# Optimization experiments

Measured on AMD Instinct MI355X. Metric: run time of the kernel, lower is better.

## Reference

```python
import jax, jax.numpy as jnp
import numpy as np

B, T, N, D = 16, 12, 2048, 128  # T*D == 12*hidden_dim, D == hidden_dim (structural constraint)


def _lin(key, out_dim, in_dim):
    k1, k2 = jax.random.split(key)
    s = 1.0 / np.sqrt(in_dim)
    W = jax.random.uniform(k1, (out_dim, in_dim), jnp.float32, -s, s)
    b = jax.random.uniform(k2, (out_dim,), jnp.float32, -s, s)
    return W, b


def setup_inputs() -> dict:
    key = jax.random.key(0)
    ks = jax.random.split(key, 12)
    x = jax.random.normal(ks[0], (B, T, N, D), jnp.float32)
    Wd1, bd1 = _lin(ks[1], D, 12 * D)      # conv_down[0] (1x1 conv == linear over channels)
    Wd2, bd2 = _lin(ks[2], D, D)           # conv_down[3]
    Wq, bq = _lin(ks[3], D, D)
    Wk, bk = _lin(ks[4], D, D)
    Wv, bv = _lin(ks[5], D, D)
    Wu1, bu1 = _lin(ks[6], 12 * D, D)      # conv_up[0]
    Wu2, bu2 = _lin(ks[7], 12 * D, 12 * D) # conv_up[3]
    gamma = jnp.ones((D,), jnp.float32)
    beta = jnp.zeros((D,), jnp.float32)
    Wr1, br1 = _lin(ks[8], D, D)
    Wr2, br2 = _lin(ks[9], D, D)
    Wi1, bi1 = _lin(ks[10], D, D)
    Wi2, bi2 = _lin(ks[11], D, D)
    return dict(x=x, Wd1=Wd1, bd1=bd1, Wd2=Wd2, bd2=bd2, Wq=Wq, bq=bq, Wk=Wk, bk=bk,
                Wv=Wv, bv=bv, Wu1=Wu1, bu1=bu1, Wu2=Wu2, bu2=bu2, gamma=gamma, beta=beta,
                Wr1=Wr1, br1=br1, Wr2=Wr2, br2=br2, Wi1=Wi1, bi1=bi1, Wi2=Wi2, bi2=bi2)


def _mlp(x, W1, b1, W2, b2):
    # Linear -> GELU(exact, torch default) -> (Dropout=identity in eval) -> Linear
    return jax.nn.gelu(x @ W1.T + b1, approximate=False) @ W2.T + b2


def reference(x, Wd1, bd1, Wd2, bd2, Wq, bq, Wk, bk, Wv, bv, Wu1, bu1, Wu2, bu2,
              gamma, beta, Wr1, br1, Wr2, br2, Wi1, bi1, Wi2, bi2):
    Bx, Tx, Nx, d = x.shape
    # ---- node self-attention branch ----
    xt = jnp.transpose(x, (0, 2, 1, 3)).reshape(Bx, Nx, Tx * d)        # [B,N,T*d]
    y = jax.nn.relu(xt @ Wd1.T + bd1) @ Wd2.T + bd2                     # conv_down: [B,N,d]
    q = y @ Wq.T + bq
    k = y @ Wk.T + bk
    v = y @ Wv.T + bv
    scale = 1.0 / jnp.sqrt(jnp.float32(d // 2))                         # dk = hidden_dim // 2
    scores = jax.nn.softmax(jnp.einsum('bnd,bmd->bnm', q, k) * scale, axis=-1)
    o = jnp.einsum('bnm,bmd->bnd', scores, v)                           # [B,N,d]
    o = jax.nn.relu(o @ Wu1.T + bu1) @ Wu2.T + bu2                      # conv_up: [B,N,12d]
    out_node = jnp.transpose(o.reshape(Bx, Nx, Tx, d), (0, 2, 1, 3))    # [B,T,N,d]
    # ---- residual + LayerNorm ----
    h1 = out_node + x
    mu = jnp.mean(h1, axis=-1, keepdims=True)
    var = jnp.mean(jnp.square(h1 - mu), axis=-1, keepdims=True)
    hn = (h1 - mu) / jnp.sqrt(var + 1e-5) * gamma + beta
    # ---- FFT dual-path MLP over time axis ----
    hf = jnp.fft.rfft(hn, axis=1)                                        # [B,T//2+1,N,d] complex
    re, im = jnp.real(hf), jnp.imag(hf)
    hr = _mlp(re, Wr1, br1, Wr2, br2) - _mlp(im, Wi1, bi1, Wi2, bi2)
    hi = _mlp(re, Wi1, bi1, Wi2, bi2) + _mlp(im, Wr1, br1, Wr2, br2)
    hc = jax.lax.complex(hr, hi)
    out = jnp.fft.irfft(hc, n=Tx, axis=1) + x
    return out
```

## Files before the change

### kernel.cpp

```cpp
#include <hip/hip_runtime.h>
#include <math.h>

#define T_ 12
#define N_ 2048
#define D_ 128
#define ND_ 262144
#define TND_ 3145728L

typedef __attribute__((ext_vector_type(8))) short short8;
typedef __attribute__((ext_vector_type(4))) float f32x4;
typedef union { float4 v; float a[4]; } f4u;

__device__ __forceinline__ ushort f2b(float f) {
  unsigned u = __float_as_uint(f);
  u += 0x7fffu + ((u >> 16) & 1u);
  return (ushort)(u >> 16);
}
__device__ __forceinline__ float b2f(ushort s) {
  return __uint_as_float(((unsigned)s) << 16);
}

__device__ __forceinline__ void gload16(const ushort* g, ushort* lds) {
  __builtin_amdgcn_global_load_lds(
      (const __attribute__((address_space(1))) void*)g,
      (__attribute__((address_space(3))) void*)lds, 16, 0, 0);
}

__constant__ float COS12[12] = {
    1.0f, 0.8660254037844387f, 0.5f, 0.0f, -0.5f, -0.8660254037844387f,
    -1.0f, -0.8660254037844387f, -0.5f, 0.0f, 0.5f, 0.8660254037844387f};
__constant__ float SIN12[12] = {
    0.0f, 0.5f, 0.8660254037844387f, 1.0f, 0.8660254037844387f, 0.5f,
    0.0f, -0.5f, -0.8660254037844387f, -1.0f, -0.8660254037844387f, -0.5f};

template <int ACT, int OUT>
__global__ __launch_bounds__(256) void mgemm(
    const ushort* __restrict__ A, const ushort* __restrict__ B,
    const float* __restrict__ bias, void* __restrict__ Cv,
    int K, int lda, int ldb, int ldc, float alpha,
    long sAb, long sBb, long sCb, int off0, int off1) {
  __shared__ ushort As[4096];
  __shared__ ushort Bs[4096];
  const int tid = threadIdx.x;
  const int w = tid >> 6;
  const int l = tid & 63;
  const int lr = l & 15;
  const int lg = l >> 4;
  const int row0 = blockIdx.y * 128;
  const int col0 = blockIdx.x * 128;
  const ushort* Ap = A + sAb * blockIdx.z;
  const ushort* Bp = B + sBb * blockIdx.z;

  f32x4 acc[2][8];
#pragma unroll
  for (int i = 0; i < 2; ++i)
#pragma unroll
    for (int j = 0; j < 8; ++j) acc[i][j] = (f32x4){0.f, 0.f, 0.f, 0.f};

  const int ba = w, bb2 = w + 4;
  const ushort* Apl = Ap + (long)(row0 + ba * 16 + lr) * lda + lg * 8;
  const ushort* Apl2 = Ap + (long)(row0 + bb2 * 16 + lr) * lda + lg * 8;
  const ushort* Bpl = Bp + (long)(col0 + ba * 16 + lr) * ldb + lg * 8;
  const ushort* Bpl2 = Bp + (long)(col0 + bb2 * 16 + lr) * ldb + lg * 8;
  for (int k0 = 0; k0 < K; k0 += 32) {
    gload16(Apl + k0, As + ba * 512);
    gload16(Apl2 + k0, As + bb2 * 512);
    gload16(Bpl + k0, Bs + ba * 512);
    gload16(Bpl2 + k0, Bs + bb2 * 512);
    __syncthreads();
    const short8 a0 = *(const short8*)(As + (w * 2 + 0) * 512 + l * 8);
    const short8 a1 = *(const short8*)(As + (w * 2 + 1) * 512 + l * 8);
#pragma unroll
    for (int ni = 0; ni < 8; ++ni) {
      const short8 bfr = *(const short8*)(Bs + ni * 512 + l * 8);
      acc[0][ni] = __builtin_amdgcn_mfma_f32_16x16x32_bf16(a0, bfr, acc[0][ni], 0, 0, 0);
      acc[1][ni] = __builtin_amdgcn_mfma_f32_16x16x32_bf16(a1, bfr, acc[1][ni], 0, 0, 0);
    }
    __syncthreads();
  }

  const long Cz = sCb * blockIdx.z;
#pragma unroll
  for (int mi = 0; mi < 2; ++mi) {
    const int grow0 = row0 + w * 32 + mi * 16 + lg * 4;
    if (OUT == 2) {
      ushort* C = (ushort*)Cv;
#pragma unroll
      for (int ni = 0; ni < 8; ++ni) {
        const int c = col0 + ni * 16 + lr;
        const float bv = bias ? bias[c] : 0.f;
        ushort4 pk;
        float v0 = acc[mi][ni][0] * alpha + bv;
        float v1 = acc[mi][ni][1] * alpha + bv;
        float v2 = acc[mi][ni][2] * alpha + bv;
        float v3 = acc[mi][ni][3] * alpha + bv;
        if (ACT == 1) { v0 = fmaxf(v0, 0.f); v1 = fmaxf(v1, 0.f); v2 = fmaxf(v2, 0.f); v3 = fmaxf(v3, 0.f); }
        pk.x = f2b(v0); pk.y = f2b(v1); pk.z = f2b(v2); pk.w = f2b(v3);
        *(ushort4*)(C + (long)c * ldc + grow0) = pk;
      }
    } else {
#pragma unroll
      for (int ni = 0; ni < 8; ++ni) {
        const int c = col0 + ni * 16 + lr;
        const float bv = bias ? bias[c] : 0.f;
        const int cm = c + (c < 128 ? off0 : off1);
#pragma unroll
        for (int r = 0; r < 4; ++r) {
          float v = acc[mi][ni][r] * alpha + bv;
          if (ACT == 1) v = fmaxf(v, 0.f);
          if (ACT == 2) v = 0.5f * v * (1.0f + erff(v * 0.7071067811865475f));
          const long off = Cz + (long)(grow0 + r) * ldc + cm;
          if (OUT == 0) ((float*)Cv)[off] = v;
          else ((ushort*)Cv)[off] = f2b(v);
        }
      }
    }
  }
}

__global__ __launch_bounds__(256) void mgemm_ln(
    const ushort* __restrict__ A, const ushort* __restrict__ B,
    const float* __restrict__ bias, const float* __restrict__ x,
    const float* __restrict__ gamma, const float* __restrict__ beta,
    float* __restrict__ hn) {
  const int K = 1536;
  __shared__ ushort As[4096];
  __shared__ ushort Bs[4096];
  const int tid = threadIdx.x;
  const int w = tid >> 6;
  const int l = tid & 63;
  const int lr = l & 15;
  const int lg = l >> 4;
  const int row0 = blockIdx.y * 128;
  const int t = blockIdx.x;
  const int col0 = t * 128;

  f32x4 acc[2][8];
#pragma unroll
  for (int i = 0; i < 2; ++i)
#pragma unroll
    for (int j = 0; j < 8; ++j) acc[i][j] = (f32x4){0.f, 0.f, 0.f, 0.f};

  const int ba = w, bb2 = w + 4;
  const ushort* Apl = A + (long)(row0 + ba * 16 + lr) * K + lg * 8;
  const ushort* Apl2 = A + (long)(row0 + bb2 * 16 + lr) * K + lg * 8;
  const ushort* Bpl = B + (long)(col0 + ba * 16 + lr) * K + lg * 8;
  const ushort* Bpl2 = B + (long)(col0 + bb2 * 16 + lr) * K + lg * 8;
  for (int k0 = 0; k0 < K; k0 += 32) {
    gload16(Apl + k0, As + ba * 512);
    gload16(Apl2 + k0, As + bb2 * 512);
    gload16(Bpl + k0, Bs + ba * 512);
    gload16(Bpl2 + k0, Bs + bb2 * 512);
    __syncthreads();
    const short8 a0 = *(const short8*)(As + (w * 2 + 0) * 512 + l * 8);
    const short8 a1 = *(const short8*)(As + (w * 2 + 1) * 512 + l * 8);
#pragma unroll
    for (int ni = 0; ni < 8; ++ni) {
      const short8 bfr = *(const short8*)(Bs + ni * 512 + l * 8);
      acc[0][ni] = __builtin_amdgcn_mfma_f32_16x16x32_bf16(a0, bfr, acc[0][ni], 0, 0, 0);
      acc[1][ni] = __builtin_amdgcn_mfma_f32_16x16x32_bf16(a1, bfr, acc[1][ni], 0, 0, 0);
    }
    __syncthreads();
  }

#pragma unroll
  for (int mi = 0; mi < 2; ++mi) {
#pragma unroll
    for (int r = 0; r < 4; ++r) {
      const int gr = row0 + w * 32 + mi * 16 + lg * 4 + r;
      const int bb = gr >> 11;
      const int nn = gr & 2047;
      const long base = ((long)(bb * 12 + t) << 18) + (long)nn * 128;
      float h[8];
      float s1 = 0.f, s2 = 0.f;
#pragma unroll
      for (int ni = 0; ni < 8; ++ni) {
        const int d = ni * 16 + lr;
        const float v = acc[mi][ni][r] + bias[col0 + d] + x[base + d];
        h[ni] = v;
        s1 += v;
        s2 += v * v;
      }
#pragma unroll
      for (int m = 1; m < 16; m <<= 1) {
        s1 += __shfl_xor(s1, m);
        s2 += __shfl_xor(s2, m);
      }
      const float mu = s1 * (1.f / 128.f);
      const float rstd = rsqrtf(s2 * (1.f / 128.f) - mu * mu + 1e-5f);
#pragma unroll
      for (int ni = 0; ni < 8; ++ni) {
        const int d = ni * 16 + lr;
        hn[base + d] = (h[ni] - mu) * rstd * gamma[d] + beta[d];
      }
    }
  }
}

__global__ __launch_bounds__(256) void softmax_k(const float* __restrict__ S,
                                                 ushort* __restrict__ P) {
  const long row = ((long)blockIdx.y * N_ + blockIdx.x) * N_;
  const int tid = threadIdx.x;
  const int w = tid >> 6;
  f4u va, vb;
  va.v = *(const float4*)(S + row + tid * 8);
  vb.v = *(const float4*)(S + row + tid * 8 + 4);
  float v[8];
#pragma unroll
  for (int j = 0; j < 4; ++j) { v[j] = va.a[j]; v[j + 4] = vb.a[j]; }
  float mx = v[0];
#pragma unroll
  for (int j = 1; j < 8; ++j) mx = fmaxf(mx, v[j]);
#pragma unroll
  for (int m = 1; m < 64; m <<= 1) mx = fmaxf(mx, __shfl_xor(mx, m));
  __shared__ float redm[4], reds[4];
  if ((tid & 63) == 0) redm[w] = mx;
  __syncthreads();
  mx = fmaxf(fmaxf(redm[0], redm[1]), fmaxf(redm[2], redm[3]));
  float sum = 0.0f;
#pragma unroll
  for (int j = 0; j < 8; ++j) {
    v[j] = expf(v[j] - mx);
    sum += v[j];
  }
#pragma unroll
  for (int m = 1; m < 64; m <<= 1) sum += __shfl_xor(sum, m);
  if ((tid & 63) == 0) reds[w] = sum;
  __syncthreads();
  const float inv = 1.0f / (reds[0] + reds[1] + reds[2] + reds[3]);
  short8 o;
#pragma unroll
  for (int j = 0; j < 8; ++j) o[j] = (short)f2b(v[j] * inv);
  *(short8*)(P + row + tid * 8) = o;
}

__global__ __launch_bounds__(256) void rfft_k(const float* __restrict__ hn,
                                              ushort* __restrict__ re,
                                              ushort* __restrict__ im) {
  const long i = (long)blockIdx.x * 256 + threadIdx.x;
  const int bb = (int)(i >> 16);
  const int nd = (int)(i & 65535) * 4;
  f4u ht[12];
#pragma unroll
  for (int t = 0; t < 12; ++t)
    ht[t].v = *(const float4*)(hn + ((long)(bb * T_ + t) << 18) + nd);
#pragma unroll
  for (int f = 0; f < 7; ++f) {
    float sr[4] = {0.f, 0.f, 0.f, 0.f}, si[4] = {0.f, 0.f, 0.f, 0.f};
#pragma unroll
    for (int t = 0; t < 12; ++t) {
      const int k = (f * t) % 12;
      const float ck = COS12[k], sk = SIN12[k];
#pragma unroll
      for (int c = 0; c < 4; ++c) {
        sr[c] = fmaf(ht[t].a[c], ck, sr[c]);
        si[c] = fmaf(ht[t].a[c], sk, si[c]);
      }
    }
    const long off = ((long)(bb * 7 + f) << 18) + nd;
    ushort4 pr, pi;
    pr.x = f2b(sr[0]); pr.y = f2b(sr[1]); pr.z = f2b(sr[2]); pr.w = f2b(sr[3]);
    pi.x = f2b(-si[0]); pi.y = f2b(-si[1]); pi.z = f2b(-si[2]); pi.w = f2b(-si[3]);
    *(ushort4*)(re + off) = pr;
    *(ushort4*)(im + off) = pi;
  }
}

__global__ __launch_bounds__(256) void irfft_k(const float* __restrict__ hr,
                                               const float* __restrict__ hi,
                                               const float* __restrict__ x,
                                               float* __restrict__ out) {
  const long i = (long)blockIdx.x * 256 + threadIdx.x;
  const int bb = (int)(i >> 16);
  const int nd = (int)(i & 65535) * 4;
  f4u r[7], m[7];
#pragma unroll
  for (int f = 0; f < 7; ++f) {
    const long off = ((long)(bb * 7 + f) << 18) + nd;
    r[f].v = *(const float4*)(hr + off);
    m[f].v = *(const float4*)(hi + off);
  }
#pragma unroll
  for (int t = 0; t < 12; ++t) {
    const long xi = ((long)(bb * T_ + t) << 18) + nd;
    f4u xv;
    xv.v = *(const float4*)(x + xi);
    f4u s;
#pragma unroll
    for (int c = 0; c < 4; ++c)
      s.a[c] = r[0].a[c] + ((t & 1) ? -r[6].a[c] : r[6].a[c]);
#pragma unroll
    for (int f = 1; f < 6; ++f) {
      const int k = (f * t) % 12;
      const float ck = 2.0f * COS12[k], sk = 2.0f * SIN12[k];
#pragma unroll
      for (int c = 0; c < 4; ++c)
        s.a[c] += r[f].a[c] * ck - m[f].a[c] * sk;
    }
#pragma unroll
    for (int c = 0; c < 4; ++c) s.a[c] = s.a[c] * (1.0f / 12.0f) + xv.a[c];
    *(float4*)(out + xi) = s.v;
  }
}

__global__ __launch_bounds__(256) void xt_k(const float* __restrict__ x,
                                            ushort* __restrict__ xt) {
  const long i = (long)blockIdx.x * 256 + threadIdx.x;
  const int d8 = (int)(i & 15) * 8;
  const long rr = i >> 4;
  const int nn = (int)(rr & 2047);
  const long r2 = rr >> 11;
  const int t = (int)(r2 % 12);
  const int bb = (int)(r2 / 12);
  f4u a, b;
  a.v = *(const float4*)(x + i * 8);
  b.v = *(const float4*)(x + i * 8 + 4);
  short8 o;
#pragma unroll
  for (int j = 0; j < 4; ++j) {
    o[j] = (short)f2b(a.a[j]);
    o[j + 4] = (short)f2b(b.a[j]);
  }
  *(short8*)(xt + ((long)bb * 2048 + nn) * 1536 + t * 128 + d8) = o;
}

__global__ __launch_bounds__(256) void prep_k(
    const float* Wd1, const float* Wd2, const float* Wq, const float* Wk,
    const float* Wv, const float* Wu1, const float* Wu2, const float* Wr1,
    const float* Wr2, const float* Wi1, const float* Wi2,
    const float* bq, const float* bk, const float* br1, const float* bi1,
    const float* br2, const float* bi2,
    ushort* __restrict__ wws, float* __restrict__ bws) {
  const long i = (long)blockIdx.x * 256 + threadIdx.x;
  if (i < 256) bws[i] = (i < 128) ? bq[i] : bk[i - 128];
  else if (i < 512) { const int j = i - 256; bws[i] = (j < 128) ? br1[j] : bi1[j - 128]; }
  else if (i < 768) { const int j = i - 512; bws[i] = (j < 128) ? bi1[j] : br1[j - 128]; }
  else if (i < 896) { const int j = i - 768; bws[i] = br2[j] - bi2[j]; }
  else if (i < 1024) { const int j = i - 896; bws[i] = bi2[j] + br2[j]; }
  if (i >= 2949120) return;
  float v;
  if (i < 196608) v = Wd1[i];
  else if (i < 212992) v = Wd2[i - 196608];
  else if (i < 245760) { const long j = i - 212992; v = (j < 16384) ? Wq[j] : Wk[j - 16384]; }
  else if (i < 262144) v = Wv[i - 245760];
  else if (i < 458752) v = Wu1[i - 262144];
  else if (i < 2818048) v = Wu2[i - 458752];
  else if (i < 2850816) { const long j = i - 2818048; v = (j < 16384) ? Wr1[j] : Wi1[j - 16384]; }
  else if (i < 2883584) { const long j = i - 2850816; v = (j < 16384) ? Wi1[j] : Wr1[j - 16384]; }
  else if (i < 2916352) {
    const long j = i - 2883584; const int n = (int)(j >> 8), k = (int)(j & 255);
    v = (k < 128) ? Wr2[n * 128 + k] : -Wi2[n * 128 + k - 128];
  } else {
    const long j = i - 2916352; const int n = (int)(j >> 8), k = (int)(j & 255);
    v = (k < 128) ? Wi2[n * 128 + k] : Wr2[n * 128 + k - 128];
  }
  wws[i] = f2b(v);
}

extern "C" void kernel_launch(void* const* d_in, const int* in_sizes, int n_in,
                              void* d_out, int out_size, void* d_ws,
                              size_t ws_size, hipStream_t stream) {
  (void)in_sizes; (void)n_in; (void)out_size;
  const float* x   = (const float*)d_in[0];
  const float* Wd1 = (const float*)d_in[1];
  const float* bd1 = (const float*)d_in[2];
  const float* Wd2 = (const float*)d_in[3];
  const float* bd2 = (const float*)d_in[4];
  const float* Wq  = (const float*)d_in[5];
  const float* bq  = (const float*)d_in[6];
  const float* Wk  = (const float*)d_in[7];
  const float* bk  = (const float*)d_in[8];
  const float* Wv  = (const float*)d_in[9];
  const float* bv  = (const float*)d_in[10];
  const float* Wu1 = (const float*)d_in[11];
  const float* bu1 = (const float*)d_in[12];
  const float* Wu2 = (const float*)d_in[13];
  const float* bu2 = (const float*)d_in[14];
  const float* gamma = (const float*)d_in[15];
  const float* beta  = (const float*)d_in[16];
  const float* Wr1 = (const float*)d_in[17];
  const float* br1 = (const float*)d_in[18];
  const float* Wr2 = (const float*)d_in[19];
  const float* br2 = (const float*)d_in[20];
  const float* Wi1 = (const float*)d_in[21];
  const float* bi1 = (const float*)d_in[22];
  const float* Wi2 = (const float*)d_in[23];
  const float* bi2 = (const float*)d_in[24];
  float* out = (float*)d_out;

  float* bws = (float*)d_ws;
  ushort* wws = (ushort*)(bws + 1024);
  const size_t kFixed = 1024 * 4 + 2949120 * 2;
  const size_t kPerBatch = 90177536;
  int CB = 1;
  const int cands[5] = {16, 8, 4, 2, 1};
  for (int ci = 0; ci < 5; ++ci)
    if (kFixed + (size_t)cands[ci] * kPerBatch <= ws_size) { CB = cands[ci]; break; }

  char* base = (char*)d_ws + kFixed;
  const long R = (long)CB * N_;
  const long Fr = (long)CB * 7 * N_;
  ushort* xt  = (ushort*)base;
  ushort* y1  = xt  + CB * 3145728L;
  ushort* y   = y1  + R * 128;
  ushort* qkb = y   + R * 128;
  ushort* vT  = qkb + R * 256;
  ushort* P   = vT  + R * 128;
  ushort* o   = P   + (long)CB * N_ * N_;
  ushort* u1  = o   + R * 128;
  ushort* re  = u1  + R * 1536;
  ushort* im  = re  + Fr * 128;
  ushort* G   = im  + Fr * 128;
  float*  S   = (float*)(G + Fr * 512);
  float*  hn  = S   + (long)CB * N_ * N_;
  float*  hr  = hn  + R * 1536;
  float*  hi  = hr  + Fr * 128;

  const dim3 blk(256);
  const float scale = 0.125f;

  prep_k<<<dim3(11520), blk, 0, stream>>>(Wd1, Wd2, Wq, Wk, Wv, Wu1, Wu2,
                                          Wr1, Wr2, Wi1, Wi2, bq, bk, br1,
                                          bi1, br2, bi2, wws, bws);
  ushort* Wd1b = wws;
  ushort* Wd2b = wws + 196608;
  ushort* Wqkb = wws + 212992;
  ushort* Wvb  = wws + 245760;
  ushort* Wu1b = wws + 262144;
  ushort* Wu2b = wws + 458752;
  ushort* W13b = wws + 2818048;
  ushort* W24b = wws + 2850816;
  ushort* Whrb = wws + 2883584;
  ushort* Whib = wws + 2916352;
  float* bqk = bws;
  float* b13 = bws + 256;
  float* b24 = bws + 512;
  float* bhr = bws + 768;
  float* bhi = bws + 896;

  for (int c = 0; c < 16 / CB; ++c) {
    const int b0 = c * CB;
    const float* xc = x + (long)b0 * TND_;
    float* oc = out + (long)b0 * TND_;
    const int GY = CB * 16;
    const int GF = CB * 112;

    xt_k<<<dim3(CB * 1536), blk, 0, stream>>>(xc, xt);
    mgemm<1, 1><<<dim3(1, GY), blk, 0, stream>>>(
        xt, Wd1b, bd1, y1, 1536, 1536, 1536, 128, 1.f, 0, 0, 0, 0, 0);
    mgemm<0, 1><<<dim3(1, GY), blk, 0, stream>>>(
        y1, Wd2b, bd2, y, 128, 128, 128, 128, 1.f, 0, 0, 0, 0, 0);
    mgemm<0, 1><<<dim3(2, GY), blk, 0, stream>>>(
        y, Wqkb, bqk, qkb, 128, 128, 128, 256, 1.f, 0, 0, 0, 0, 0);
    mgemm<0, 2><<<dim3(1, GY), blk, 0, stream>>>(
        y, Wvb, bv, vT, 128, 128, 128, (int)R, 1.f, 0, 0, 0, 0, 0);
    mgemm<0, 0><<<dim3(16, 16, CB), blk, 0, stream>>>(
        qkb, qkb + 128, nullptr, S, 128, 256, 256, 2048, scale,
        524288, 524288, 4194304, 0, 0);
    softmax_k<<<dim3(N_, CB), blk, 0, stream>>>(S, P);
    mgemm<0, 1><<<dim3(1, 16, CB), blk, 0, stream>>>(
        P, vT, nullptr, o, 2048, 2048, (int)R, 128, 1.f,
        4194304, 2048, 262144, 0, 0);
    mgemm<1, 1><<<dim3(12, GY), blk, 0, stream>>>(
        o, Wu1b, bu1, u1, 128, 128, 128, 1536, 1.f, 0, 0, 0, 0, 0);
    mgemm_ln<<<dim3(12, GY), blk, 0, stream>>>(u1, Wu2b, bu2, xc, gamma, beta, hn);
    rfft_k<<<dim3(CB * 256), blk, 0, stream>>>(hn, re, im);
    mgemm<2, 1><<<dim3(2, GF), blk, 0, stream>>>(
        re, W13b, b13, G, 128, 128, 128, 512, 1.f, 0, 0, 0, 0, 128);
    mgemm<2, 1><<<dim3(2, GF), blk, 0, stream>>>(
        im, W24b, b24, G, 128, 128, 128, 512, 1.f, 0, 0, 0, 128, 256);
    mgemm<0, 0><<<dim3(1, GF), blk, 0, stream>>>(
        G, Whrb, bhr, hr, 256, 512, 256, 128, 1.f, 0, 0, 0, 0, 0);
    mgemm<0, 0><<<dim3(1, GF), blk, 0, stream>>>(
        G + 256, Whib, bhi, hi, 256, 512, 256, 128, 1.f, 0, 0, 0, 0, 0);
    irfft_k<<<dim3(CB * 256), blk, 0, stream>>>(hr, hi, xc, oc);
  }
}
```

Before: 1.785 ms.

## Fuse attention into flash-style kernel and fold x transpose into down-projection GEMM

Replaces the QK^T GEMM, the separate softmax kernel and the PV GEMM with a single online-softmax attention kernel that keeps scores in registers and LDS, so the fp32 score matrix and bf16 probability matrix are never written to or read from global memory. The x transpose/convert kernel is also removed: the first down-projection GEMM now reads fp32 x directly and converts it to bf16 in registers. Risks include lower parallelism in attention (16 blocks per batch), K/V fragments read straight from global memory without LDS staging, and uncoalesced A loads in the fused down-projection.

```diff
diff --git a/kernel.cpp b/kernel.cpp
--- a/kernel.cpp
+++ b/kernel.cpp
@@ -9,7 +9,9 @@
 
 typedef __attribute__((ext_vector_type(8))) short short8;
 typedef __attribute__((ext_vector_type(4))) float f32x4;
+typedef __attribute__((ext_vector_type(4))) unsigned int u32x4;
 typedef union { float4 v; float a[4]; } f4u;
+typedef union { short8 s8; u32x4 u; } frag_u;
 
 __device__ __forceinline__ ushort f2b(float f) {
   unsigned u = __float_as_uint(f);
@@ -118,6 +120,76 @@
   }
 }
 
+__global__ __launch_bounds__(256) void mgemm_xa(
+    const float* __restrict__ x, const ushort* __restrict__ B,
+    const float* __restrict__ bias, ushort* __restrict__ C) {
+  __shared__ ushort Bs[4096];
+  const int tid = threadIdx.x;
+  const int w = tid >> 6;
+  const int l = tid & 63;
+  const int lr = l & 15;
+  const int lg = l >> 4;
+  const int row0 = blockIdx.y * 128;
+  const int b = row0 >> 11;
+  const int nn0 = row0 & 2047;
+
+  f32x4 acc[2][8];
+#pragma unroll
+  for (int i = 0; i < 2; ++i)
+#pragma unroll
+    for (int j = 0; j < 8; ++j) acc[i][j] = (f32x4){0.f, 0.f, 0.f, 0.f};
+
+  const int ba = w, bb2 = w + 4;
+  const ushort* Bpl = B + (long)(ba * 16 + lr) * 1536 + lg * 8;
+  const ushort* Bpl2 = B + (long)(bb2 * 16 + lr) * 1536 + lg * 8;
+  const long ar0 = (long)(nn0 + w * 32 + 0 * 16 + lr) * 128;
+  const long ar1 = (long)(nn0 + w * 32 + 1 * 16 + lr) * 128;
+
+  for (int k0 = 0; k0 < 1536; k0 += 32) {
+    const int t = k0 >> 7;
+    const int df = (k0 & 127) + lg * 8;
+    const float* xt_ = x + (((long)(b * 12 + t)) << 18) + df;
+    f4u p0, p1, q0, q1;
+    p0.v = *(const float4*)(xt_ + ar0);
+    p1.v = *(const float4*)(xt_ + ar0 + 4);
+    q0.v = *(const float4*)(xt_ + ar1);
+    q1.v = *(const float4*)(xt_ + ar1 + 4);
+    frag_u a0, a1;
+#pragma unroll
+    for (int j = 0; j < 4; ++j) {
+      a0.u[j] = (unsigned)f2b(j < 2 ? p0.a[2 * j] : p1.a[2 * j - 4]) |
+                ((unsigned)f2b(j < 2 ? p0.a[2 * j + 1] : p1.a[2 * j - 3]) << 16);
+      a1.u[j] = (unsigned)f2b(j < 2 ? q0.a[2 * j] : q1.a[2 * j - 4]) |
+                ((unsigned)f2b(j < 2 ? q0.a[2 * j + 1] : q1.a[2 * j - 3]) << 16);
+    }
+    gload16(Bpl + k0, Bs + ba * 512);
+    gload16(Bpl2 + k0, Bs + bb2 * 512);
+    __syncthreads();
+#pragma unroll
+    for (int ni = 0; ni < 8; ++ni) {
+      const short8 bfr = *(const short8*)(Bs + ni * 512 + l * 8);
+      acc[0][ni] = __builtin_amdgcn_mfma_f32_16x16x32_bf16(a0.s8, bfr, acc[0][ni], 0, 0, 0);
+      acc[1][ni] = __builtin_amdgcn_mfma_f32_16x16x32_bf16(a1.s8, bfr, acc[1][ni], 0, 0, 0);
+    }
+    __syncthreads();
+  }
+
+#pragma unroll
+  for (int mi = 0; mi < 2; ++mi) {
+    const int grow0 = row0 + w * 32 + mi * 16 + lg * 4;
+#pragma unroll
+    for (int ni = 0; ni < 8; ++ni) {
+      const int c = ni * 16 + lr;
+      const float bv = bias[c];
+#pragma unroll
+      for (int r = 0; r < 4; ++r) {
+        float v = fmaxf(acc[mi][ni][r] + bv, 0.f);
+        C[(long)(grow0 + r) * 128 + c] = f2b(v);
+      }
+    }
+  }
+}
+
 __global__ __launch_bounds__(256) void mgemm_ln(
     const ushort* __restrict__ A, const ushort* __restrict__ B,
     const float* __restrict__ bias, const float* __restrict__ x,
@@ -197,41 +269,113 @@
   }
 }
 
-__global__ __launch_bounds__(256) void softmax_k(const float* __restrict__ S,
-                                                 ushort* __restrict__ P) {
-  const long row = ((long)blockIdx.y * N_ + blockIdx.x) * N_;
+__global__ __launch_bounds__(256) void attn_k(
+    const ushort* __restrict__ qkb,
+    const ushort* __restrict__ vT,
+    ushort* __restrict__ o,
+    long R) {
+  __shared__ __align__(16) ushort Pl[4][32][136];
   const int tid = threadIdx.x;
   const int w = tid >> 6;
-  f4u va, vb;
-  va.v = *(const float4*)(S + row + tid * 8);
-  vb.v = *(const float4*)(S + row + tid * 8 + 4);
-  float v[8];
-#pragma unroll
-  for (int j = 0; j < 4; ++j) { v[j] = va.a[j]; v[j + 4] = vb.a[j]; }
-  float mx = v[0];
-#pragma unroll
-  for (int j = 1; j < 8; ++j) mx = fmaxf(mx, v[j]);
-#pragma unroll
-  for (int m = 1; m < 64; m <<= 1) mx = fmaxf(mx, __shfl_xor(mx, m));
-  __shared__ float redm[4], reds[4];
-  if ((tid & 63) == 0) redm[w] = mx;
-  __syncthreads();
-  mx = fmaxf(fmaxf(redm[0], redm[1]), fmaxf(redm[2], redm[3]));
-  float sum = 0.0f;
-#pragma unroll
-  for (int j = 0; j < 8; ++j) {
-    v[j] = expf(v[j] - mx);
-    sum += v[j];
-  }
-#pragma unroll
-  for (int m = 1; m < 64; m <<= 1) sum += __shfl_xor(sum, m);
-  if ((tid & 63) == 0) reds[w] = sum;
-  __syncthreads();
-  const float inv = 1.0f / (reds[0] + reds[1] + reds[2] + reds[3]);
-  short8 o;
-#pragma unroll
-  for (int j = 0; j < 8; ++j) o[j] = (short)f2b(v[j] * inv);
-  *(short8*)(P + row + tid * 8) = o;
+  const int l = tid & 63;
+  const int lr = l & 15;
+  const int lg = l >> 4;
+  const long zrow = (long)blockIdx.y * 2048;
+  const int row0 = blockIdx.x * 128 + w * 32;
+
+  frag_u qf[2][4];
+#pragma unroll
+  for (int f = 0; f < 2; ++f)
+#pragma unroll
+    for (int kc = 0; kc < 4; ++kc)
+      qf[f][kc].u = *(const u32x4*)(qkb + (zrow + row0 + f * 16 + lr) * 256 + kc * 32 + lg * 8);
+
+  f32x4 oa[2][8];
+#pragma unroll
+  for (int i = 0; i < 2; ++i)
+#pragma unroll
+    for (int j = 0; j < 8; ++j) oa[i][j] = (f32x4){0.f, 0.f, 0.f, 0.f};
+  float mrow[2][4], lrow[2][4];
+#pragma unroll
+  for (int i = 0; i < 2; ++i)
+#pragma unroll
+    for (int r = 0; r < 4; ++r) { mrow[i][r] = -3.4e38f; lrow[i][r] = 0.f; }
+
+#pragma unroll 1
+  for (int kt = 0; kt < 16; ++kt) {
+    const long kbase = zrow + kt * 128;
+    f32x4 s[2][8];
+#pragma unroll
+    for (int i = 0; i < 2; ++i)
+#pragma unroll
+      for (int j = 0; j < 8; ++j) s[i][j] = (f32x4){0.f, 0.f, 0.f, 0.f};
+#pragma unroll
+    for (int kc = 0; kc < 4; ++kc) {
+#pragma unroll
+      for (int ni = 0; ni < 8; ++ni) {
+        frag_u kf;
+        kf.u = *(const u32x4*)(qkb + (kbase + ni * 16 + lr) * 256 + 128 + kc * 32 + lg * 8);
+        s[0][ni] = __builtin_amdgcn_mfma_f32_16x16x32_bf16(qf[0][kc].s8, kf.s8, s[0][ni], 0, 0, 0);
+        s[1][ni] = __builtin_amdgcn_mfma_f32_16x16x32_bf16(qf[1][kc].s8, kf.s8, s[1][ni], 0, 0, 0);
+      }
+    }
+#pragma unroll
+    for (int mi = 0; mi < 2; ++mi) {
+#pragma unroll
+      for (int r = 0; r < 4; ++r) {
+        float mx = s[mi][0][r];
+#pragma unroll
+        for (int ni = 1; ni < 8; ++ni) mx = fmaxf(mx, s[mi][ni][r]);
+#pragma unroll
+        for (int msk = 1; msk < 16; msk <<= 1) mx = fmaxf(mx, __shfl_xor(mx, msk));
+        mx *= 0.125f;
+        const float mnew = fmaxf(mrow[mi][r], mx);
+        const float psc = expf(mrow[mi][r] - mnew);
+        mrow[mi][r] = mnew;
+        float psum = 0.f;
+#pragma unroll
+        for (int ni = 0; ni < 8; ++ni) {
+          const float p = expf(fmaf(s[mi][ni][r], 0.125f, -mnew));
+          s[mi][ni][r] = p;
+          psum += p;
+        }
+#pragma unroll
+        for (int msk = 1; msk < 16; msk <<= 1) psum += __shfl_xor(psum, msk);
+        lrow[mi][r] = lrow[mi][r] * psc + psum;
+#pragma unroll
+        for (int ni = 0; ni < 8; ++ni) oa[mi][ni][r] *= psc;
+        const int q = mi * 16 + lg * 4 + r;
+#pragma unroll
+        for (int ni = 0; ni < 8; ++ni)
+          Pl[w][q][ni * 16 + lr] = f2b(s[mi][ni][r]);
+      }
+    }
+#pragma unroll
+    for (int kc = 0; kc < 4; ++kc) {
+      frag_u pa0, pa1;
+      pa0.s8 = *(const short8*)(&Pl[w][lr][kc * 32 + lg * 8]);
+      pa1.s8 = *(const short8*)(&Pl[w][16 + lr][kc * 32 + lg * 8]);
+#pragma unroll
+      for (int ni = 0; ni < 8; ++ni) {
+        frag_u vf;
+        vf.u = *(const u32x4*)(vT + (long)(ni * 16 + lr) * R + kbase + kc * 32 + lg * 8);
+        oa[0][ni] = __builtin_amdgcn_mfma_f32_16x16x32_bf16(pa0.s8, vf.s8, oa[0][ni], 0, 0, 0);
+        oa[1][ni] = __builtin_amdgcn_mfma_f32_16x16x32_bf16(pa1.s8, vf.s8, oa[1][ni], 0, 0, 0);
+      }
+    }
+  }
+
+#pragma unroll
+  for (int mi = 0; mi < 2; ++mi) {
+#pragma unroll
+    for (int r = 0; r < 4; ++r) {
+      const float inv = 1.0f / lrow[mi][r];
+      const long grow = zrow + row0 + mi * 16 + lg * 4 + r;
+#pragma unroll
+      for (int ni = 0; ni < 8; ++ni)
+        o[grow * 128 + ni * 16 + lr] = f2b(oa[mi][ni][r] * inv);
+    }
+  }
 }
 
 __global__ __launch_bounds__(256) void rfft_k(const float* __restrict__ hn,
@@ -301,27 +445,6 @@
     for (int c = 0; c < 4; ++c) s.a[c] = s.a[c] * (1.0f / 12.0f) + xv.a[c];
     *(float4*)(out + xi) = s.v;
   }
-}
-
-__global__ __launch_bounds__(256) void xt_k(const float* __restrict__ x,
-                                            ushort* __restrict__ xt) {
-  const long i = (long)blockIdx.x * 256 + threadIdx.x;
-  const int d8 = (int)(i & 15) * 8;
-  const long rr = i >> 4;
-  const int nn = (int)(rr & 2047);
-  const long r2 = rr >> 11;
-  const int t = (int)(r2 % 12);
-  const int bb = (int)(r2 / 12);
-  f4u a, b;
-  a.v = *(const float4*)(x + i * 8);
-  b.v = *(const float4*)(x + i * 8 + 4);
-  short8 o;
-#pragma unroll
-  for (int j = 0; j < 4; ++j) {
-    o[j] = (short)f2b(a.a[j]);
-    o[j + 4] = (short)f2b(b.a[j]);
-  }
-  *(short8*)(xt + ((long)bb * 2048 + nn) * 1536 + t * 128 + d8) = o;
 }
 
 __global__ __launch_bounds__(256) void prep_k(
@@ -417,7 +540,6 @@
   float*  hi  = hr  + Fr * 128;
 
   const dim3 blk(256);
-  const float scale = 0.125f;
 
   prep_k<<<dim3(11520), blk, 0, stream>>>(Wd1, Wd2, Wq, Wk, Wv, Wu1, Wu2,
                                           Wr1, Wr2, Wi1, Wi2, bq, bk, br1,
@@ -445,22 +567,14 @@
     const int GY = CB * 16;
     const int GF = CB * 112;
 
-    xt_k<<<dim3(CB * 1536), blk, 0, stream>>>(xc, xt);
-    mgemm<1, 1><<<dim3(1, GY), blk, 0, stream>>>(
-        xt, Wd1b, bd1, y1, 1536, 1536, 1536, 128, 1.f, 0, 0, 0, 0, 0);
+    mgemm_xa<<<dim3(1, GY), blk, 0, stream>>>(xc, Wd1b, bd1, y1);
     mgemm<0, 1><<<dim3(1, GY), blk, 0, stream>>>(
         y1, Wd2b, bd2, y, 128, 128, 128, 128, 1.f, 0, 0, 0, 0, 0);
     mgemm<0, 1><<<dim3(2, GY), blk, 0, stream>>>(
         y, Wqkb, bqk, qkb, 128, 128, 128, 256, 1.f, 0, 0, 0, 0, 0);
     mgemm<0, 2><<<dim3(1, GY), blk, 0, stream>>>(
         y, Wvb, bv, vT, 128, 128, 128, (int)R, 1.f, 0, 0, 0, 0, 0);
-    mgemm<0, 0><<<dim3(16, 16, CB), blk, 0, stream>>>(
-        qkb, qkb + 128, nullptr, S, 128, 256, 256, 2048, scale,
-        524288, 524288, 4194304, 0, 0);
-    softmax_k<<<dim3(N_, CB), blk, 0, stream>>>(S, P);
-    mgemm<0, 1><<<dim3(1, 16, CB), blk, 0, stream>>>(
-        P, vT, nullptr, o, 2048, 2048, (int)R, 128, 1.f,
-        4194304, 2048, 262144, 0, 0);
+    attn_k<<<dim3(16, CB), blk, 0, stream>>>(qkb, vT, o, R);
     mgemm<1, 1><<<dim3(12, GY), blk, 0, stream>>>(
         o, Wu1b, bu1, u1, 128, 128, 128, 1536, 1.f, 0, 0, 0, 0, 0);
     mgemm_ln<<<dim3(12, GY), blk, 0, stream>>>(u1, Wu2b, bu2, xc, gamma, beta, hn);
```

Result: slower. 1.984 ms (+11.1%).
